# Optimization experiments

Hardware: AMD Instinct MI355X
Metric: run time of the kernel (lower is better)

Reference implementation:

```python
import jax, jax.numpy as jnp
import numpy as np

N, C, A, H, O, T = 18, 4, 14, 20, 8, 5  # nodes, classes, alarms, hidden, out, time steps


def _lin(key, dout, din, std):
    W = std * jax.random.normal(key, (dout, din), jnp.float32)
    b = jnp.zeros((dout,), jnp.float32)
    return W, b


def setup_inputs():
    key = jax.random.key(0)
    ks = jax.random.split(key, 12)
    adj = (jax.random.uniform(ks[0], (N, N)) < 0.3).astype(jnp.float32)  # binary adjacency
    x = jax.random.normal(ks[1], (N, H), jnp.float32)
    Wz, bz = _lin(ks[2], H, 2 * H, 0.1)
    Uz, buz = _lin(ks[3], H, H, 0.1)
    Wr, br = _lin(ks[4], H, 2 * H, 0.1)
    Ur, bur = _lin(ks[5], H, H, 0.1)
    Ww, bw = _lin(ks[6], H, 2 * H, 0.1)
    Uw, bu = _lin(ks[7], H, H, 0.1)
    Wo, bo = _lin(ks[8], O, 2 * H, 0.1)
    Wx, bx = _lin(ks[9], O, H, 0.01)
    Wy, by = _lin(ks[10], O, H, 0.01)
    w2, b2 = _lin(ks[11], 1, O, 0.1)
    return {"x": x, "adj": adj, "Wz": Wz, "bz": bz, "Uz": Uz, "buz": buz,
            "Wr": Wr, "br": br, "Ur": Ur, "bur": bur, "Ww": Ww, "bw": bw,
            "Uw": Uw, "bu": bu, "Wo": Wo, "bo": bo, "Wx": Wx, "bx": bx,
            "Wy": Wy, "by": by, "w2": w2, "b2": b2}


def reference(x, adj, Wz, bz, Uz, buz, Wr, br, Ur, bur, Ww, bw, Uw, bu,
              Wo, bo, Wx, bx, Wy, by, w2, b2):
    in_mat, out_mat = adj, adj.T  # split_matrix: in=A, out=A^T

    def step(h, _):
        # message aggregation over in/out edges, then GRU gates (eqs 3-5)
        a = jnp.concatenate([in_mat @ h, out_mat @ h], axis=1)        # [N, 2H]
        z = jax.nn.sigmoid(a @ Wz.T + bz + h @ Uz.T + buz)            # update gate
        r = jax.nn.sigmoid(a @ Wr.T + br + h @ Ur.T + bur)            # reset gate
        hg = jnp.tanh(a @ Ww.T + bw + (r * h) @ Uw.T + bu)            # candidate
        return (1.0 - z) * h + z * hg, None

    h, _ = jax.lax.scan(step, x, None, length=T)                       # [N, H]
    out = jnp.tanh(jnp.concatenate([h, x], axis=1) @ Wo.T + bo)        # [N, O]

    # attention-style reasoning between class nodes and alarm nodes
    cfcx = jnp.tanh(h[:C] @ Wx.T + bx)                                 # [C, O]
    afcy = jnp.tanh(h[C:] @ Wy.T + by)                                 # [A, O]
    cacat = cfcx[:, None, :] * afcy[None, :, :]                        # [C, A, O]
    rfc = jax.nn.sigmoid(jnp.einsum('cao,o->ca', cacat, w2[0]) + b2[0])[..., None]
    mask = in_mat[:C, C:][..., None]                                   # [C, A, 1]
    rfc = rfc * mask

    weighted = out[C:][None, :, :] * rfc                               # [C, A, O]
    final = jnp.concatenate([out[:C][:, None, :], weighted], axis=1)   # [C, 1+A, O]
    return final
```

## Files before the change

kernel.cpp:

```cpp
#include <hip/hip_runtime.h>


#define AS 44

__device__ __forceinline__ float fsig(float x){ return 1.0f/(1.0f+__expf(-x)); }
__device__ __forceinline__ float ftnh(float x){ return 1.0f - 2.0f/(__expf(2.0f*x)+1.0f); }

__global__ __launch_bounds__(384, 1) void ggnn_fused(
    const float* __restrict__ x,  const float* __restrict__ adj,
    const float* __restrict__ Wz, const float* __restrict__ bz,
    const float* __restrict__ Uz, const float* __restrict__ buz,
    const float* __restrict__ Wr, const float* __restrict__ br,
    const float* __restrict__ Ur, const float* __restrict__ bur,
    const float* __restrict__ Ww, const float* __restrict__ bw,
    const float* __restrict__ Uw, const float* __restrict__ bu,
    const float* __restrict__ Wo, const float* __restrict__ bo,
    const float* __restrict__ Wx, const float* __restrict__ bx,
    const float* __restrict__ Wy, const float* __restrict__ by,
    const float* __restrict__ w2, const float* __restrict__ b2,
    float* __restrict__ outp)
{
  __shared__ __align__(16) float hA[360], hB[360];
  __shared__ __align__(16) float aaL[18*AS];
  __shared__ __align__(16) float rrL[360];
  __shared__ float sAdj[324];
  __shared__ __align__(16) float sOut[144], sCf[32], sAf[112], sRfc[56];

  const int tid = threadIdx.x;

  const bool act2 = (tid < 360);
  const int i2 = tid / 18;
  const int n2 = tid % 18;

  const bool act1 = (tid < 180);
  const int n1 = tid / 10;
  const int q1 = tid % 10;
  const int hoff1 = 4 * (q1 % 5);

  if (tid < 90) ((float4*)hA)[tid] = ((const float4*)x)[tid];
  if (tid < 324) sAdj[tid] = adj[tid];

  float adjv[18];
  if (act1) {
    #pragma unroll
    for (int m = 0; m < 18; ++m)
      adjv[m] = (q1 < 5) ? adj[n1*18 + m] : adj[m*18 + n1];
  }

  float4 wz4[10], wr4[10], ww4[10], uz4[5], ur4[5], uw4[5];
  float bzz=0.f, brr=0.f, bww=0.f, bui=0.f;
  if (act2) {
    #pragma unroll
    for (int q=0;q<10;q++){
      wz4[q] = ((const float4*)(Wz + i2*40))[q];
      wr4[q] = ((const float4*)(Wr + i2*40))[q];
      ww4[q] = ((const float4*)(Ww + i2*40))[q];
    }
    #pragma unroll
    for (int q=0;q<5;q++){
      uz4[q] = ((const float4*)(Uz + i2*20))[q];
      ur4[q] = ((const float4*)(Ur + i2*20))[q];
      uw4[q] = ((const float4*)(Uw + i2*20))[q];
    }
    bzz = bz[i2] + buz[i2];
    brr = br[i2] + bur[i2];
    bww = bw[i2];
    bui = bu[i2];
  }
  __syncthreads();

  float* hc = hA;
  float* hn = hB;
  float zreg = 0.f, swreg = 0.f;

  for (int t = 0; t < 5; ++t) {
    if (act1) {
      float4 acc = make_float4(0.f,0.f,0.f,0.f);
      #pragma unroll
      for (int m = 0; m < 18; ++m) {
        float4 h4 = *(const float4*)&hc[m*20 + hoff1];
        float av = adjv[m];
        acc.x += av*h4.x; acc.y += av*h4.y; acc.z += av*h4.z; acc.w += av*h4.w;
      }
      *(float4*)&aaL[n1*AS + 4*q1] = acc;
    }
    __syncthreads();

    if (act2) {
      float sz = bzz, sr = brr, sw = bww;
      const float4* ar = (const float4*)&aaL[n2*AS];
      #pragma unroll
      for (int q=0;q<10;q++){
        float4 a4 = ar[q];
        sz += wz4[q].x*a4.x + wz4[q].y*a4.y + wz4[q].z*a4.z + wz4[q].w*a4.w;
        sr += wr4[q].x*a4.x + wr4[q].y*a4.y + wr4[q].z*a4.z + wr4[q].w*a4.w;
        sw += ww4[q].x*a4.x + ww4[q].y*a4.y + ww4[q].z*a4.z + ww4[q].w*a4.w;
      }
      const float4* hr = (const float4*)&hc[n2*20];
      #pragma unroll
      for (int q=0;q<5;q++){
        float4 h4 = hr[q];
        sz += uz4[q].x*h4.x + uz4[q].y*h4.y + uz4[q].z*h4.z + uz4[q].w*h4.w;
        sr += ur4[q].x*h4.x + ur4[q].y*h4.y + ur4[q].z*h4.z + ur4[q].w*h4.w;
      }
      zreg  = fsig(sz);
      swreg = sw;
      rrL[n2*20 + i2] = fsig(sr);
    }
    __syncthreads();

    if (act2) {
      float s = swreg + bui;
      const float4* rr4 = (const float4*)&rrL[n2*20];
      const float4* hr  = (const float4*)&hc[n2*20];
      #pragma unroll
      for (int q=0;q<5;q++){
        float4 r4 = rr4[q];
        float4 h4 = hr[q];
        s += uw4[q].x*r4.x*h4.x + uw4[q].y*r4.y*h4.y
           + uw4[q].z*r4.z*h4.z + uw4[q].w*r4.w*h4.w;
      }
      float hg = ftnh(s);
      float hv = hc[n2*20 + i2];
      hn[n2*20 + i2] = (1.f - zreg)*hv + zreg*hg;
    }
    __syncthreads();
    float* tmp = hc; hc = hn; hn = tmp;
  }

  if (tid < 144) {
    int n_ = tid/8, o = tid%8;
    const float4* hr = (const float4*)&hc[n_*20];
    const float4* wo = (const float4*)(Wo + o*40);
    const float4* xv = (const float4*)(x + n_*20);
    float s = bo[o];
    #pragma unroll
    for (int q=0;q<5;q++){
      float4 w = wo[q],  h4 = hr[q];
      s += w.x*h4.x + w.y*h4.y + w.z*h4.z + w.w*h4.w;
      float4 w2_ = wo[5+q], x4 = xv[q];
      s += w2_.x*x4.x + w2_.y*x4.y + w2_.z*x4.z + w2_.w*x4.w;
    }
    sOut[tid] = ftnh(s);
  } else if (tid >= 144 && tid < 176) {
    int ii = tid-144; int c = ii/8, o = ii%8;
    const float4* hr = (const float4*)&hc[c*20];
    const float4* wx = (const float4*)(Wx + o*20);
    float s = bx[o];
    #pragma unroll
    for (int q=0;q<5;q++){
      float4 w = wx[q], h4 = hr[q];
      s += w.x*h4.x + w.y*h4.y + w.z*h4.z + w.w*h4.w;
    }
    sCf[ii] = ftnh(s);
  } else if (tid >= 176 && tid < 288) {
    int ii = tid-176; int a = ii/8, o = ii%8;
    const float4* hr = (const float4*)&hc[(4+a)*20];
    const float4* wy = (const float4*)(Wy + o*20);
    float s = by[o];
    #pragma unroll
    for (int q=0;q<5;q++){
      float4 w = wy[q], h4 = hr[q];
      s += w.x*h4.x + w.y*h4.y + w.z*h4.z + w.w*h4.w;
    }
    sAf[ii] = ftnh(s);
  }
  __syncthreads();

  if (tid < 56) {
    int c = tid/14, a = tid%14;
    float4 w20 = ((const float4*)w2)[0];
    float4 w21 = ((const float4*)w2)[1];
    const float* cf = &sCf[c*8];
    const float* af = &sAf[a*8];
    float s = b2[0];
    s += cf[0]*af[0]*w20.x + cf[1]*af[1]*w20.y + cf[2]*af[2]*w20.z + cf[3]*af[3]*w20.w;
    s += cf[4]*af[4]*w21.x + cf[5]*af[5]*w21.y + cf[6]*af[6]*w21.z + cf[7]*af[7]*w21.w;
    sRfc[tid] = fsig(s) * sAdj[c*18 + 4 + a];
  }
  __syncthreads();

  for (int o = tid; o < 480; o += 384) {
    int c = o/120, rem = o%120, s_ = rem/8, oo = rem%8;
    float v = (s_ == 0) ? sOut[c*8+oo]
                        : sOut[(3+s_)*8+oo] * sRfc[c*14 + (s_-1)];
    outp[o] = v;
  }
}

extern "C" void kernel_launch(void* const* d_in, const int* in_sizes, int n_in,
                              void* d_out, int out_size, void* d_ws, size_t ws_size,
                              hipStream_t stream) {
  (void)in_sizes; (void)n_in; (void)d_ws; (void)ws_size; (void)out_size;
  const float* x   = (const float*)d_in[0];
  const float* adj = (const float*)d_in[1];
  const float* Wz  = (const float*)d_in[2];
  const float* bz  = (const float*)d_in[3];
  const float* Uz  = (const float*)d_in[4];
  const float* buz = (const float*)d_in[5];
  const float* Wr  = (const float*)d_in[6];
  const float* br  = (const float*)d_in[7];
  const float* Ur  = (const float*)d_in[8];
  const float* bur = (const float*)d_in[9];
  const float* Ww  = (const float*)d_in[10];
  const float* bw  = (const float*)d_in[11];
  const float* Uw  = (const float*)d_in[12];
  const float* bu  = (const float*)d_in[13];
  const float* Wo  = (const float*)d_in[14];
  const float* bo  = (const float*)d_in[15];
  const float* Wx  = (const float*)d_in[16];
  const float* bx  = (const float*)d_in[17];
  const float* Wy  = (const float*)d_in[18];
  const float* by  = (const float*)d_in[19];
  const float* w2  = (const float*)d_in[20];
  const float* b2  = (const float*)d_in[21];
  float* outp = (float*)d_out;

  ggnn_fused<<<1, 384, 0, stream>>>(x, adj, Wz, bz, Uz, buz, Wr, br, Ur, bur,
                                    Ww, bw, Uw, bu, Wo, bo, Wx, bx, Wy, by,
                                    w2, b2, outp);
}
```

Measured before the change: 23.80 us.

## Split GRU gate work across twice the threads and transpose h for aggregation

```diff
diff --git a/kernel.cpp b/kernel.cpp
--- a/kernel.cpp
+++ b/kernel.cpp
@@ -2,11 +2,15 @@
 
 
 #define AS 44
+#define HS 20
 
 __device__ __forceinline__ float fsig(float x){ return 1.0f/(1.0f+__expf(-x)); }
 __device__ __forceinline__ float ftnh(float x){ return 1.0f - 2.0f/(__expf(2.0f*x)+1.0f); }
-
-__global__ __launch_bounds__(384, 1) void ggnn_fused(
+__device__ __forceinline__ float dot4(float4 a, float4 b){
+  return a.x*b.x + a.y*b.y + a.z*b.z + a.w*b.w;
+}
+
+__global__ __launch_bounds__(768, 3) void ggnn_fused(
     const float* __restrict__ x,  const float* __restrict__ adj,
     const float* __restrict__ Wz, const float* __restrict__ bz,
     const float* __restrict__ Uz, const float* __restrict__ buz,
@@ -20,99 +24,109 @@
     const float* __restrict__ w2, const float* __restrict__ b2,
     float* __restrict__ outp)
 {
-  __shared__ __align__(16) float hA[360], hB[360];
-  __shared__ __align__(16) float aaL[18*AS];
-  __shared__ __align__(16) float rrL[360];
   __shared__ float sAdj[324];
+  __shared__ __align__(16) float hT[20*HS];
+  __shared__ __align__(16) float hRA[18*HS], hRB[18*HS];
+  __shared__ __align__(16) float aaR[18*AS];
+  __shared__ __align__(16) float rrR[18*HS];
+  __shared__ float ws1[18*HS];
   __shared__ __align__(16) float sOut[144], sCf[32], sAf[112], sRfc[56];
 
   const int tid = threadIdx.x;
 
-  const bool act2 = (tid < 360);
-  const int i2 = tid / 18;
-  const int n2 = tid % 18;
-
-  const bool act1 = (tid < 180);
-  const int n1 = tid / 10;
-  const int q1 = tid % 10;
-  const int hoff1 = 4 * (q1 % 5);
-
-  if (tid < 90) ((float4*)hA)[tid] = ((const float4*)x)[tid];
+  const int g   = (tid >> 6) & 1;
+  const int idx = (tid >> 7) * 64 + (tid & 63);
+  const bool act2 = (idx < 360);
+  const int i2 = idx / 18, n2 = idx % 18;
+
+  const bool act1 = (tid < 720);
+  const int n1 = tid % 18;
+  const int kk = tid / 18;
+  const int k1 = (kk < 20) ? kk : (kk - 20);
+
   if (tid < 324) sAdj[tid] = adj[tid];
+  if (tid < 90)  ((float4*)hRA)[tid] = ((const float4*)x)[tid];
+  if (tid < 360) { int j = tid/18, n = tid%18; hT[j*HS+n] = x[n*20+j]; }
 
   float adjv[18];
   if (act1) {
     #pragma unroll
     for (int m = 0; m < 18; ++m)
-      adjv[m] = (q1 < 5) ? adj[n1*18 + m] : adj[m*18 + n1];
-  }
-
-  float4 wz4[10], wr4[10], ww4[10], uz4[5], ur4[5], uw4[5];
-  float bzz=0.f, brr=0.f, bww=0.f, bui=0.f;
+      adjv[m] = (kk < 20) ? adj[n1*18 + m] : adj[m*18 + n1];
+  }
+
+  float4 w4[10], wh4[5], u4[5], uw4[5];
+  float bias1 = 0.f, bwi = 0.f, bui = 0.f;
   if (act2) {
-    #pragma unroll
-    for (int q=0;q<10;q++){
-      wz4[q] = ((const float4*)(Wz + i2*40))[q];
-      wr4[q] = ((const float4*)(Wr + i2*40))[q];
-      ww4[q] = ((const float4*)(Ww + i2*40))[q];
-    }
+    const float* Wg = g ? Wr : Wz;
+    const float* Ug = g ? Ur : Uz;
+    #pragma unroll
+    for (int q=0;q<10;q++) w4[q] = *(const float4*)(Wg + i2*40 + 4*q);
     #pragma unroll
     for (int q=0;q<5;q++){
-      uz4[q] = ((const float4*)(Uz + i2*20))[q];
-      ur4[q] = ((const float4*)(Ur + i2*20))[q];
-      uw4[q] = ((const float4*)(Uw + i2*20))[q];
-    }
-    bzz = bz[i2] + buz[i2];
-    brr = br[i2] + bur[i2];
-    bww = bw[i2];
-    bui = bu[i2];
+      u4[q]  = *(const float4*)(Ug + i2*20 + 4*q);
+      wh4[q] = *(const float4*)(Ww + i2*40 + g*20 + 4*q);
+    }
+    if (g == 0){
+      bias1 = bz[i2] + buz[i2];
+      bwi   = bw[i2];
+      bui   = bu[i2];
+      #pragma unroll
+      for (int q=0;q<5;q++) uw4[q] = *(const float4*)(Uw + i2*20 + 4*q);
+    } else {
+      bias1 = br[i2] + bur[i2];
+    }
   }
   __syncthreads();
 
-  float* hc = hA;
-  float* hn = hB;
+  float* hc = hRA;
+  float* hn = hRB;
   float zreg = 0.f, swreg = 0.f;
 
   for (int t = 0; t < 5; ++t) {
     if (act1) {
-      float4 acc = make_float4(0.f,0.f,0.f,0.f);
-      #pragma unroll
-      for (int m = 0; m < 18; ++m) {
-        float4 h4 = *(const float4*)&hc[m*20 + hoff1];
-        float av = adjv[m];
-        acc.x += av*h4.x; acc.y += av*h4.y; acc.z += av*h4.z; acc.w += av*h4.w;
+      const float* hrow = &hT[k1*HS];
+      float4 t0 = *(const float4*)(hrow + 0);
+      float4 t1 = *(const float4*)(hrow + 4);
+      float4 t2 = *(const float4*)(hrow + 8);
+      float4 t3 = *(const float4*)(hrow + 12);
+      float  ta = hrow[16], tb = hrow[17];
+      float s = 0.f;
+      s += adjv[0]*t0.x + adjv[1]*t0.y + adjv[2]*t0.z + adjv[3]*t0.w;
+      s += adjv[4]*t1.x + adjv[5]*t1.y + adjv[6]*t1.z + adjv[7]*t1.w;
+      s += adjv[8]*t2.x + adjv[9]*t2.y + adjv[10]*t2.z + adjv[11]*t2.w;
+      s += adjv[12]*t3.x + adjv[13]*t3.y + adjv[14]*t3.z + adjv[15]*t3.w;
+      s += adjv[16]*ta + adjv[17]*tb;
+      aaR[n1*AS + kk] = s;
+    }
+    __syncthreads();
+
+    if (act2) {
+      const float4* ar = (const float4*)&aaR[n2*AS];
+      const float4* hr = (const float4*)&hc[n2*HS];
+      float sg = bias1;
+      #pragma unroll
+      for (int q=0;q<10;q++) sg += dot4(w4[q], ar[q]);
+      #pragma unroll
+      for (int q=0;q<5;q++)  sg += dot4(u4[q], hr[q]);
+      const float4* arw = ar + (g ? 5 : 0);
+      float sw = bwi;
+      #pragma unroll
+      for (int q=0;q<5;q++)  sw += dot4(wh4[q], arw[q]);
+      if (g == 0){
+        zreg  = fsig(sg);
+        swreg = sw;
+      } else {
+        rrR[n2*HS + i2] = fsig(sg);
+        ws1[n2*HS + i2] = sw;
       }
-      *(float4*)&aaL[n1*AS + 4*q1] = acc;
     }
     __syncthreads();
 
-    if (act2) {
-      float sz = bzz, sr = brr, sw = bww;
-      const float4* ar = (const float4*)&aaL[n2*AS];
-      #pragma unroll
-      for (int q=0;q<10;q++){
-        float4 a4 = ar[q];
-        sz += wz4[q].x*a4.x + wz4[q].y*a4.y + wz4[q].z*a4.z + wz4[q].w*a4.w;
-        sr += wr4[q].x*a4.x + wr4[q].y*a4.y + wr4[q].z*a4.z + wr4[q].w*a4.w;
-        sw += ww4[q].x*a4.x + ww4[q].y*a4.y + ww4[q].z*a4.z + ww4[q].w*a4.w;
-      }
-      const float4* hr = (const float4*)&hc[n2*20];
-      #pragma unroll
-      for (int q=0;q<5;q++){
-        float4 h4 = hr[q];
-        sz += uz4[q].x*h4.x + uz4[q].y*h4.y + uz4[q].z*h4.z + uz4[q].w*h4.w;
-        sr += ur4[q].x*h4.x + ur4[q].y*h4.y + ur4[q].z*h4.z + ur4[q].w*h4.w;
-      }
-      zreg  = fsig(sz);
-      swreg = sw;
-      rrL[n2*20 + i2] = fsig(sr);
-    }
-    __syncthreads();
-
-    if (act2) {
-      float s = swreg + bui;
-      const float4* rr4 = (const float4*)&rrL[n2*20];
-      const float4* hr  = (const float4*)&hc[n2*20];
+    if (g == 0 && act2) {
+      float s = swreg + ws1[n2*HS + i2] + bui;
+      const float4* rr4 = (const float4*)&rrR[n2*HS];
+      const float4* hr  = (const float4*)&hc[n2*HS];
       #pragma unroll
       for (int q=0;q<5;q++){
         float4 r4 = rr4[q];
@@ -121,8 +135,10 @@
            + uw4[q].z*r4.z*h4.z + uw4[q].w*r4.w*h4.w;
       }
       float hg = ftnh(s);
-      float hv = hc[n2*20 + i2];
-      hn[n2*20 + i2] = (1.f - zreg)*hv + zreg*hg;
+      float hv = hc[n2*HS + i2];
+      float hnv = (1.f - zreg)*hv + zreg*hg;
+      hn[n2*HS + i2] = hnv;
+      hT[i2*HS + n2] = hnv;
     }
     __syncthreads();
     float* tmp = hc; hc = hn; hn = tmp;
@@ -130,39 +146,31 @@
 
   if (tid < 144) {
     int n_ = tid/8, o = tid%8;
-    const float4* hr = (const float4*)&hc[n_*20];
+    const float4* hr = (const float4*)&hc[n_*HS];
     const float4* wo = (const float4*)(Wo + o*40);
     const float4* xv = (const float4*)(x + n_*20);
     float s = bo[o];
     #pragma unroll
     for (int q=0;q<5;q++){
-      float4 w = wo[q],  h4 = hr[q];
-      s += w.x*h4.x + w.y*h4.y + w.z*h4.z + w.w*h4.w;
-      float4 w2_ = wo[5+q], x4 = xv[q];
-      s += w2_.x*x4.x + w2_.y*x4.y + w2_.z*x4.z + w2_.w*x4.w;
+      s += dot4(wo[q],   hr[q]);
+      s += dot4(wo[5+q], xv[q]);
     }
     sOut[tid] = ftnh(s);
   } else if (tid >= 144 && tid < 176) {
     int ii = tid-144; int c = ii/8, o = ii%8;
-    const float4* hr = (const float4*)&hc[c*20];
+    const float4* hr = (const float4*)&hc[c*HS];
     const float4* wx = (const float4*)(Wx + o*20);
     float s = bx[o];
     #pragma unroll
-    for (int q=0;q<5;q++){
-      float4 w = wx[q], h4 = hr[q];
-      s += w.x*h4.x + w.y*h4.y + w.z*h4.z + w.w*h4.w;
-    }
+    for (int q=0;q<5;q++) s += dot4(wx[q], hr[q]);
     sCf[ii] = ftnh(s);
   } else if (tid >= 176 && tid < 288) {
     int ii = tid-176; int a = ii/8, o = ii%8;
-    const float4* hr = (const float4*)&hc[(4+a)*20];
+    const float4* hr = (const float4*)&hc[(4+a)*HS];
     const float4* wy = (const float4*)(Wy + o*20);
     float s = by[o];
     #pragma unroll
-    for (int q=0;q<5;q++){
-      float4 w = wy[q], h4 = hr[q];
-      s += w.x*h4.x + w.y*h4.y + w.z*h4.z + w.w*h4.w;
-    }
+    for (int q=0;q<5;q++) s += dot4(wy[q], hr[q]);
     sAf[ii] = ftnh(s);
   }
   __syncthreads();
@@ -180,11 +188,11 @@
   }
   __syncthreads();
 
-  for (int o = tid; o < 480; o += 384) {
-    int c = o/120, rem = o%120, s_ = rem/8, oo = rem%8;
+  if (tid < 480) {
+    int c = tid/120, rem = tid%120, s_ = rem/8, oo = rem%8;
     float v = (s_ == 0) ? sOut[c*8+oo]
                         : sOut[(3+s_)*8+oo] * sRfc[c*14 + (s_-1)];
-    outp[o] = v;
+    outp[tid] = v;
   }
 }
 
@@ -216,7 +224,7 @@
   const float* b2  = (const float*)d_in[21];
   float* outp = (float*)d_out;
 
-  ggnn_fused<<<1, 384, 0, stream>>>(x, adj, Wz, bz, Uz, buz, Wr, br, Ur, bur,
+  ggnn_fused<<<1, 768, 0, stream>>>(x, adj, Wz, bz, Uz, buz, Wr, br, Ur, bur,
                                     Ww, bw, Uw, bu, Wo, bo, Wx, bx, Wy, by,
                                     w2, b2, outp);
 }
```

Measured after the change: 21.27 us. 10.6% less time.

## Assign whole nodes to waves to replace block barriers with wave-local syncs

Applied to the files above, without the earlier changes.

```diff
diff --git a/kernel.cpp b/kernel.cpp
--- a/kernel.cpp
+++ b/kernel.cpp
@@ -1,10 +1,13 @@
 #include <hip/hip_runtime.h>
 
-
-#define AS 44
 
 __device__ __forceinline__ float fsig(float x){ return 1.0f/(1.0f+__expf(-x)); }
 __device__ __forceinline__ float ftnh(float x){ return 1.0f - 2.0f/(__expf(2.0f*x)+1.0f); }
+__device__ __forceinline__ float dot4(float4 a, float4 b){
+  return a.x*b.x + a.y*b.y + a.z*b.z + a.w*b.w;
+}
+#define WAVE_SYNC() do { asm volatile("s_waitcnt lgkmcnt(0)" ::: "memory"); \
+                         __builtin_amdgcn_sched_barrier(0); } while(0)
 
 __global__ __launch_bounds__(384, 1) void ggnn_fused(
     const float* __restrict__ x,  const float* __restrict__ adj,
@@ -20,149 +23,134 @@
     const float* __restrict__ w2, const float* __restrict__ b2,
     float* __restrict__ outp)
 {
-  __shared__ __align__(16) float hA[360], hB[360];
-  __shared__ __align__(16) float aaL[18*AS];
-  __shared__ __align__(16) float rrL[360];
   __shared__ float sAdj[324];
+  __shared__ __align__(16) float hR[360];
+  __shared__ __align__(16) float hT0[400], hT1[400];
+  __shared__ __align__(16) float aaR[720];
+  __shared__ __align__(16) float vR[360];
   __shared__ __align__(16) float sOut[144], sCf[32], sAf[112], sRfc[56];
 
-  const int tid = threadIdx.x;
-
-  const bool act2 = (tid < 360);
-  const int i2 = tid / 18;
-  const int n2 = tid % 18;
-
-  const bool act1 = (tid < 180);
-  const int n1 = tid / 10;
-  const int q1 = tid % 10;
-  const int hoff1 = 4 * (q1 % 5);
-
-  if (tid < 90) ((float4*)hA)[tid] = ((const float4*)x)[tid];
+  const int tid  = threadIdx.x;
+  const int lane = tid & 63;
+  const int wave = tid >> 6;
+  const bool act = (lane < 60);
+  const int n = wave*3 + lane/20;
+  const int j = lane % 20;
+
   if (tid < 324) sAdj[tid] = adj[tid];
-
-  float adjv[18];
-  if (act1) {
-    #pragma unroll
-    for (int m = 0; m < 18; ++m)
-      adjv[m] = (q1 < 5) ? adj[n1*18 + m] : adj[m*18 + n1];
-  }
-
-  float4 wz4[10], wr4[10], ww4[10], uz4[5], ur4[5], uw4[5];
-  float bzz=0.f, brr=0.f, bww=0.f, bui=0.f;
-  if (act2) {
+  if (tid < 90)  ((float4*)hR)[tid] = ((const float4*)x)[tid];
+  for (int s2 = tid; s2 < 400; s2 += 384) {
+    int jj = s2/20, mm = s2%20;
+    hT0[s2] = (mm < 18) ? x[mm*20 + jj] : 0.f;
+  }
+  if (tid < 40) { int jj = tid>>1, mm = 18 + (tid&1); hT1[jj*20+mm] = 0.f; }
+
+  float4 wz[10], wr[10], ww[10], uz[5], ur[5], uw[5];
+  float bzz=0.f, brr=0.f, bwi=0.f, bui=0.f;
+  float adin[20], adout[20];
+  if (act) {
     #pragma unroll
     for (int q=0;q<10;q++){
-      wz4[q] = ((const float4*)(Wz + i2*40))[q];
-      wr4[q] = ((const float4*)(Wr + i2*40))[q];
-      ww4[q] = ((const float4*)(Ww + i2*40))[q];
+      wz[q] = *(const float4*)(Wz + j*40 + 4*q);
+      wr[q] = *(const float4*)(Wr + j*40 + 4*q);
+      ww[q] = *(const float4*)(Ww + j*40 + 4*q);
     }
     #pragma unroll
     for (int q=0;q<5;q++){
-      uz4[q] = ((const float4*)(Uz + i2*20))[q];
-      ur4[q] = ((const float4*)(Ur + i2*20))[q];
-      uw4[q] = ((const float4*)(Uw + i2*20))[q];
-    }
-    bzz = bz[i2] + buz[i2];
-    brr = br[i2] + bur[i2];
-    bww = bw[i2];
-    bui = bu[i2];
+      uz[q] = *(const float4*)(Uz + j*20 + 4*q);
+      ur[q] = *(const float4*)(Ur + j*20 + 4*q);
+      uw[q] = *(const float4*)(Uw + j*20 + 4*q);
+    }
+    bzz = bz[j] + buz[j];
+    brr = br[j] + bur[j];
+    bwi = bw[j];
+    bui = bu[j];
+    #pragma unroll
+    for (int m=0;m<18;m++){ adin[m] = adj[n*18+m]; adout[m] = adj[m*18+n]; }
+    adin[18]=adin[19]=adout[18]=adout[19]=0.f;
   }
   __syncthreads();
 
-  float* hc = hA;
-  float* hn = hB;
-  float zreg = 0.f, swreg = 0.f;
+  const float* hTc = hT0;
+  float*       hTn = hT1;
 
   for (int t = 0; t < 5; ++t) {
-    if (act1) {
-      float4 acc = make_float4(0.f,0.f,0.f,0.f);
-      #pragma unroll
-      for (int m = 0; m < 18; ++m) {
-        float4 h4 = *(const float4*)&hc[m*20 + hoff1];
-        float av = adjv[m];
-        acc.x += av*h4.x; acc.y += av*h4.y; acc.z += av*h4.z; acc.w += av*h4.w;
+    if (act) {
+      const float* hTr = hTc + j*20;
+      float si = 0.f, so = 0.f;
+      #pragma unroll
+      for (int q=0;q<5;q++){
+        float4 h4 = *(const float4*)(hTr + 4*q);
+        si += adin[4*q+0]*h4.x + adin[4*q+1]*h4.y + adin[4*q+2]*h4.z + adin[4*q+3]*h4.w;
+        so += adout[4*q+0]*h4.x + adout[4*q+1]*h4.y + adout[4*q+2]*h4.z + adout[4*q+3]*h4.w;
       }
-      *(float4*)&aaL[n1*AS + 4*q1] = acc;
-    }
-    __syncthreads();
-
-    if (act2) {
-      float sz = bzz, sr = brr, sw = bww;
-      const float4* ar = (const float4*)&aaL[n2*AS];
+      float* ap = &aaR[n*40 + j];
+      ap[0]  = si;
+      ap[20] = so;
+      WAVE_SYNC();
+
+      const float4* ar = (const float4*)&aaR[n*40];
+      const float4* hr = (const float4*)&hR[n*20];
+      float sz = bzz, sr = brr, sw = bwi;
       #pragma unroll
       for (int q=0;q<10;q++){
         float4 a4 = ar[q];
-        sz += wz4[q].x*a4.x + wz4[q].y*a4.y + wz4[q].z*a4.z + wz4[q].w*a4.w;
-        sr += wr4[q].x*a4.x + wr4[q].y*a4.y + wr4[q].z*a4.z + wr4[q].w*a4.w;
-        sw += ww4[q].x*a4.x + ww4[q].y*a4.y + ww4[q].z*a4.z + ww4[q].w*a4.w;
+        sz += dot4(wz[q], a4);
+        sr += dot4(wr[q], a4);
+        sw += dot4(ww[q], a4);
       }
-      const float4* hr = (const float4*)&hc[n2*20];
       #pragma unroll
       for (int q=0;q<5;q++){
         float4 h4 = hr[q];
-        sz += uz4[q].x*h4.x + uz4[q].y*h4.y + uz4[q].z*h4.z + uz4[q].w*h4.w;
-        sr += ur4[q].x*h4.x + ur4[q].y*h4.y + ur4[q].z*h4.z + ur4[q].w*h4.w;
+        sz += dot4(uz[q], h4);
+        sr += dot4(ur[q], h4);
       }
-      zreg  = fsig(sz);
-      swreg = sw;
-      rrL[n2*20 + i2] = fsig(sr);
+      float hv = hR[n*20 + j];
+      float zv = fsig(sz);
+      float rv = fsig(sr);
+      vR[n*20 + j] = rv * hv;
+      WAVE_SYNC();
+
+      const float4* vr = (const float4*)&vR[n*20];
+      float s = sw + bui;
+      #pragma unroll
+      for (int q=0;q<5;q++) s += dot4(uw[q], vr[q]);
+      float hg = ftnh(s);
+      float hnv = (1.f - zv)*hv + zv*hg;
+      hR[n*20 + j]  = hnv;
+      hTn[j*20 + n] = hnv;
     }
     __syncthreads();
-
-    if (act2) {
-      float s = swreg + bui;
-      const float4* rr4 = (const float4*)&rrL[n2*20];
-      const float4* hr  = (const float4*)&hc[n2*20];
-      #pragma unroll
-      for (int q=0;q<5;q++){
-        float4 r4 = rr4[q];
-        float4 h4 = hr[q];
-        s += uw4[q].x*r4.x*h4.x + uw4[q].y*r4.y*h4.y
-           + uw4[q].z*r4.z*h4.z + uw4[q].w*r4.w*h4.w;
-      }
-      float hg = ftnh(s);
-      float hv = hc[n2*20 + i2];
-      hn[n2*20 + i2] = (1.f - zreg)*hv + zreg*hg;
-    }
-    __syncthreads();
-    float* tmp = hc; hc = hn; hn = tmp;
+    const float* tc = hTc; hTc = hTn; hTn = (float*)tc;
   }
 
   if (tid < 144) {
     int n_ = tid/8, o = tid%8;
-    const float4* hr = (const float4*)&hc[n_*20];
+    const float4* hr = (const float4*)&hR[n_*20];
     const float4* wo = (const float4*)(Wo + o*40);
     const float4* xv = (const float4*)(x + n_*20);
     float s = bo[o];
     #pragma unroll
     for (int q=0;q<5;q++){
-      float4 w = wo[q],  h4 = hr[q];
-      s += w.x*h4.x + w.y*h4.y + w.z*h4.z + w.w*h4.w;
-      float4 w2_ = wo[5+q], x4 = xv[q];
-      s += w2_.x*x4.x + w2_.y*x4.y + w2_.z*x4.z + w2_.w*x4.w;
+      s += dot4(wo[q],   hr[q]);
+      s += dot4(wo[5+q], xv[q]);
     }
     sOut[tid] = ftnh(s);
   } else if (tid >= 144 && tid < 176) {
     int ii = tid-144; int c = ii/8, o = ii%8;
-    const float4* hr = (const float4*)&hc[c*20];
+    const float4* hr = (const float4*)&hR[c*20];
     const float4* wx = (const float4*)(Wx + o*20);
     float s = bx[o];
     #pragma unroll
-    for (int q=0;q<5;q++){
-      float4 w = wx[q], h4 = hr[q];
-      s += w.x*h4.x + w.y*h4.y + w.z*h4.z + w.w*h4.w;
-    }
+    for (int q=0;q<5;q++) s += dot4(wx[q], hr[q]);
     sCf[ii] = ftnh(s);
   } else if (tid >= 176 && tid < 288) {
     int ii = tid-176; int a = ii/8, o = ii%8;
-    const float4* hr = (const float4*)&hc[(4+a)*20];
+    const float4* hr = (const float4*)&hR[(4+a)*20];
     const float4* wy = (const float4*)(Wy + o*20);
     float s = by[o];
     #pragma unroll
-    for (int q=0;q<5;q++){
-      float4 w = wy[q], h4 = hr[q];
-      s += w.x*h4.x + w.y*h4.y + w.z*h4.z + w.w*h4.w;
-    }
+    for (int q=0;q<5;q++) s += dot4(wy[q], hr[q]);
     sAf[ii] = ftnh(s);
   }
   __syncthreads();
```

Measured after the change: 20.93 us. 1.14x faster.
